# Performance work log

Measured on AMD Instinct MI355X. Metric: run time of the kernel, lower is better.

## Reference

```python
import jax, jax.numpy as jnp
import numpy as np

B, T, C = 4, 1024, 2048
H, HKV, HD = 32, 8, 64
HID = 5632  # round_up(8*2048/3, 256)
EPS = 1e-6


def rmsnorm(x, scale):
    return x * scale * jax.lax.rsqrt(jnp.mean(x * x, axis=-1, keepdims=True) + EPS)


def rotary(t, cos, sin):
    # interleaved even/odd rotation, matching torch apply_rotary_emb
    te, to = t[..., ::2], t[..., 1::2]
    return jnp.stack((te * cos - to * sin, te * sin + to * cos), axis=-1).reshape(t.shape)


def setup_inputs() -> dict:
    key = jax.random.key(0)
    ks = jax.random.split(key, 8)
    s = 0.02
    inv = 1.0 / (10000.0 ** (np.arange(0, HD, 2, dtype=np.float64) / HD))
    ang = np.arange(T, dtype=np.float64)[:, None] * inv[None, :]
    return {
        "x": jax.random.normal(ks[0], (B, T, C), jnp.float32),
        "cos": jnp.asarray(np.cos(ang), jnp.float32),
        "sin": jnp.asarray(np.sin(ang), jnp.float32),
        "w_attn": jax.random.normal(ks[1], (C, (H + 2 * HKV) * HD), jnp.float32) * s,
        "w_proj": jax.random.normal(ks[2], (C, C), jnp.float32) * s,
        "w_gate": jax.random.normal(ks[3], (C, HID), jnp.float32) * s,
        "w_up": jax.random.normal(ks[4], (C, HID), jnp.float32) * s,
        "w_down": jax.random.normal(ks[5], (HID, C), jnp.float32) * s,
        "scale1": jnp.ones((C,), jnp.float32),
        "scale2": jnp.ones((C,), jnp.float32),
    }


def reference(x, cos, sin, w_attn, w_proj, w_gate, w_up, w_down, scale1, scale2):
    n_rep = H // HKV
    # --- attention block ---
    h = rmsnorm(x, scale1)
    qkv = h @ w_attn  # [B,T,(H+2*HKV)*HD]
    q, k, v = jnp.split(qkv, [H * HD, (H + HKV) * HD], axis=-1)
    q = q.reshape(B, T, H, HD).transpose(0, 2, 1, 3)      # [B,H,T,HD]
    k = k.reshape(B, T, HKV, HD).transpose(0, 2, 1, 3)    # [B,HKV,T,HD]
    v = v.reshape(B, T, HKV, HD).transpose(0, 2, 1, 3)
    q = rotary(q, cos, sin)
    k = rotary(k, cos, sin)
    # GQA: group q heads over kv heads instead of repeat_interleave
    qg = q.reshape(B, HKV, n_rep, T, HD)
    scores = jnp.einsum('bgrtd,bgsd->bgrts', qg, k) / jnp.sqrt(jnp.float32(HD))
    causal = jnp.tril(jnp.ones((T, T), bool))
    scores = jnp.where(causal, scores, jnp.finfo(scores.dtype).min)
    p = jax.nn.softmax(scores, axis=-1)
    y = jnp.einsum('bgrts,bgsd->bgrtd', p, v)
    y = y.reshape(B, H, T, HD).transpose(0, 2, 1, 3).reshape(B, T, C)
    x = x + y @ w_proj
    # --- SwiGLU MLP block ---
    h2 = rmsnorm(x, scale2)
    x = x + (jax.nn.silu(h2 @ w_gate) * (h2 @ w_up)) @ w_down
    return x
```

## Files before the change

### kernel.cpp

```cpp
#include <hip/hip_runtime.h>
#include <stdint.h>

#define B_ 4
#define T_ 1024
#define C_ 2048
#define H_ 32
#define HKV_ 8
#define HD_ 64
#define HID_ 5632

typedef __attribute__((ext_vector_type(8))) short short8;
typedef __attribute__((ext_vector_type(4))) float floatx4;

__device__ __forceinline__ float b2f(short s) {
  unsigned u = ((unsigned)(unsigned short)s) << 16;
  return __uint_as_float(u);
}
__device__ __forceinline__ short f2b(float f) {
  unsigned u = __float_as_uint(f);
  u = u + 0x7fffu + ((u >> 16) & 1u);
  return (short)(u >> 16);
}

#define GL2LDS(gp, lp)                                              \
  __builtin_amdgcn_global_load_lds(                                 \
      (const __attribute__((address_space(1))) void*)(gp),          \
      (__attribute__((address_space(3))) void*)(lp), 16, 0, 0)

__global__ __launch_bounds__(256) void convt_kernel(
    const float* __restrict__ W, short* __restrict__ Wt, int K, int N) {
  __shared__ short t[32][33];
  int n0 = blockIdx.x * 32, k0 = blockIdx.y * 32;
  int tx = threadIdx.x & 31, ty = threadIdx.x >> 5;
#pragma unroll
  for (int j = 0; j < 4; ++j)
    t[ty + j * 8][tx] = f2b(W[(size_t)(k0 + ty + j * 8) * N + n0 + tx]);
  __syncthreads();
#pragma unroll
  for (int j = 0; j < 4; ++j)
    Wt[(size_t)(n0 + ty + j * 8) * K + k0 + tx] = t[tx][ty + j * 8];
}

__global__ __launch_bounds__(256) void rmsnorm_kernel(
    const float* __restrict__ x, const float* __restrict__ scale,
    short* __restrict__ out) {
  int row = blockIdx.x, tid = threadIdx.x;
  const float4* xr = (const float4*)(x + (size_t)row * C_);
  float4 v0 = xr[tid], v1 = xr[tid + 256];
  float s = v0.x * v0.x + v0.y * v0.y + v0.z * v0.z + v0.w * v0.w +
            v1.x * v1.x + v1.y * v1.y + v1.z * v1.z + v1.w * v1.w;
  for (int off = 32; off > 0; off >>= 1) s += __shfl_down(s, off, 64);
  __shared__ float red[4];
  if ((tid & 63) == 0) red[tid >> 6] = s;
  __syncthreads();
  float tot = red[0] + red[1] + red[2] + red[3];
  float r = rsqrtf(tot * (1.0f / (float)C_) + 1e-6f);
  const float4* sc = (const float4*)scale;
  float4 s0 = sc[tid], s1 = sc[tid + 256];
  short* o = out + (size_t)row * C_;
  o[tid * 4 + 0] = f2b(v0.x * s0.x * r);
  o[tid * 4 + 1] = f2b(v0.y * s0.y * r);
  o[tid * 4 + 2] = f2b(v0.z * s0.z * r);
  o[tid * 4 + 3] = f2b(v0.w * s0.w * r);
  o[1024 + tid * 4 + 0] = f2b(v1.x * s1.x * r);
  o[1024 + tid * 4 + 1] = f2b(v1.y * s1.y * r);
  o[1024 + tid * 4 + 2] = f2b(v1.z * s1.z * r);
  o[1024 + tid * 4 + 3] = f2b(v1.w * s1.w * r);
}

template <int EPI>
__global__ __launch_bounds__(256, 2) void gemm128_kernel(
    const short* __restrict__ A, const short* __restrict__ Bt,
    void* __restrict__ Out, const float* __restrict__ resid,
    int M, int N, int K) {
  __shared__ __align__(16) short smem[8192];
  short* As = smem;
  short* Bs = smem + 4096;
  int tid = threadIdx.x, lane = tid & 63, wave = tid >> 6;
  int quad = lane >> 4, l16 = lane & 15;
  int m0 = blockIdx.y * 128, n0 = blockIdx.x * 128;
  int wm = (wave & 1) * 64, wn = (wave >> 1) * 64;

  int SA0 = wave * 128 + lane, SA1 = SA0 + 64;
  int rA0 = SA0 >> 2, kA0 = ((SA0 & 3) - ((SA0 >> 3) & 3)) & 3;
  int rA1 = SA1 >> 2, kA1 = ((SA1 & 3) - ((SA1 >> 3) & 3)) & 3;
  const short* ap0 = A + (size_t)(m0 + rA0) * K + kA0 * 8;
  const short* ap1 = A + (size_t)(m0 + rA1) * K + kA1 * 8;
  const short* bp0 = Bt + (size_t)(n0 + rA0) * K + kA0 * 8;
  const short* bp1 = Bt + (size_t)(n0 + rA1) * K + kA1 * 8;
  short* lA0 = As + (wave * 128) * 8;
  short* lA1 = As + (wave * 128 + 64) * 8;
  short* lB0 = Bs + (wave * 128) * 8;
  short* lB1 = Bs + (wave * 128 + 64) * 8;

  int aoff[4], boff[4];
#pragma unroll
  for (int i = 0; i < 4; ++i) {
    int ra = wm + i * 16 + l16;
    aoff[i] = (ra * 4 + ((quad + (ra >> 1)) & 3)) * 8;
    int rb = wn + i * 16 + l16;
    boff[i] = (rb * 4 + ((quad + (rb >> 1)) & 3)) * 8;
  }

  floatx4 acc[4][4] = {};
  for (int k0 = 0; k0 < K; k0 += 32) {
    GL2LDS(ap0 + k0, lA0);
    GL2LDS(ap1 + k0, lA1);
    GL2LDS(bp0 + k0, lB0);
    GL2LDS(bp1 + k0, lB1);
    __syncthreads();
    short8 af[4], bf[4];
#pragma unroll
    for (int i = 0; i < 4; ++i) af[i] = *(const short8*)(As + aoff[i]);
#pragma unroll
    for (int i = 0; i < 4; ++i) bf[i] = *(const short8*)(Bs + boff[i]);
#pragma unroll
    for (int mi = 0; mi < 4; ++mi)
#pragma unroll
      for (int ni = 0; ni < 4; ++ni)
        acc[mi][ni] = __builtin_amdgcn_mfma_f32_16x16x32_bf16(
            af[mi], bf[ni], acc[mi][ni], 0, 0, 0);
    __syncthreads();
  }
#pragma unroll
  for (int mi = 0; mi < 4; ++mi)
#pragma unroll
    for (int ni = 0; ni < 4; ++ni)
#pragma unroll
      for (int r = 0; r < 4; ++r) {
        int row = m0 + wm + mi * 16 + quad * 4 + r;
        int col = n0 + wn + ni * 16 + l16;
        size_t idx = (size_t)row * N + col;
        float a = acc[mi][ni][r];
        if constexpr (EPI == 0)
          ((short*)Out)[idx] = f2b(a);
        else
          ((float*)Out)[idx] = resid[idx] + a;
      }
}

__global__ __launch_bounds__(256, 2) void gateup_kernel(
    const short* __restrict__ A, const short* __restrict__ Wg,
    const short* __restrict__ Wu, short* __restrict__ act, int K) {
  __shared__ __align__(16) short smem[8192];
  short* As = smem;
  short* Bs = smem + 4096;
  int tid = threadIdx.x, lane = tid & 63, wave = tid >> 6;
  int quad = lane >> 4, l16 = lane & 15;
  int m0 = blockIdx.y * 128, n0 = blockIdx.x * 64;
  int wm = (wave & 1) * 64, half = wave >> 1;

  int SA0 = wave * 128 + lane, SA1 = SA0 + 64;
  int rA0 = SA0 >> 2, kA0 = ((SA0 & 3) - ((SA0 >> 3) & 3)) & 3;
  int rA1 = SA1 >> 2, kA1 = ((SA1 & 3) - ((SA1 >> 3) & 3)) & 3;
  const short* ap0 = A + (size_t)(m0 + rA0) * K + kA0 * 8;
  const short* ap1 = A + (size_t)(m0 + rA1) * K + kA1 * 8;
  const short* bp0 = (rA0 < 64 ? Wg + (size_t)(n0 + rA0) * K
                               : Wu + (size_t)(n0 + rA0 - 64) * K) + kA0 * 8;
  const short* bp1 = (rA1 < 64 ? Wg + (size_t)(n0 + rA1) * K
                               : Wu + (size_t)(n0 + rA1 - 64) * K) + kA1 * 8;
  short* lA0 = As + (wave * 128) * 8;
  short* lA1 = As + (wave * 128 + 64) * 8;
  short* lB0 = Bs + (wave * 128) * 8;
  short* lB1 = Bs + (wave * 128 + 64) * 8;

  int aoff[4], boff[4];
#pragma unroll
  for (int i = 0; i < 4; ++i) {
    int ra = wm + i * 16 + l16;
    aoff[i] = (ra * 4 + ((quad + (ra >> 1)) & 3)) * 8;
    int rb = half * 64 + i * 16 + l16;
    boff[i] = (rb * 4 + ((quad + (rb >> 1)) & 3)) * 8;
  }

  floatx4 acc[4][4] = {};
  for (int k0 = 0; k0 < K; k0 += 32) {
    GL2LDS(ap0 + k0, lA0);
    GL2LDS(ap1 + k0, lA1);
    GL2LDS(bp0 + k0, lB0);
    GL2LDS(bp1 + k0, lB1);
    __syncthreads();
    short8 af[4], bf[4];
#pragma unroll
    for (int i = 0; i < 4; ++i) af[i] = *(const short8*)(As + aoff[i]);
#pragma unroll
    for (int i = 0; i < 4; ++i) bf[i] = *(const short8*)(Bs + boff[i]);
#pragma unroll
    for (int mi = 0; mi < 4; ++mi)
#pragma unroll
      for (int ni = 0; ni < 4; ++ni)
        acc[mi][ni] = __builtin_amdgcn_mfma_f32_16x16x32_bf16(
            af[mi], bf[ni], acc[mi][ni], 0, 0, 0);
    __syncthreads();
  }
  short* Ex = smem;
  if (half == 1) {
#pragma unroll
    for (int mi = 0; mi < 4; ++mi)
#pragma unroll
      for (int ni = 0; ni < 4; ++ni)
#pragma unroll
        for (int r = 0; r < 4; ++r)
          Ex[(wm + mi * 16 + quad * 4 + r) * 64 + ni * 16 + l16] =
              f2b(acc[mi][ni][r]);
  }
  __syncthreads();
  if (half == 0) {
#pragma unroll
    for (int mi = 0; mi < 4; ++mi)
#pragma unroll
      for (int ni = 0; ni < 4; ++ni)
#pragma unroll
        for (int r = 0; r < 4; ++r) {
          int row = wm + mi * 16 + quad * 4 + r;
          int col = ni * 16 + l16;
          float u = b2f(Ex[row * 64 + col]);
          float g = acc[mi][ni][r];
          float a = g / (1.0f + __expf(-g)) * u;
          act[(size_t)(m0 + row) * HID_ + n0 + col] = f2b(a);
        }
  }
}

__global__ __launch_bounds__(256) void rope_kernel(
    const short* __restrict__ qkv, const float* __restrict__ cosp,
    const float* __restrict__ sinp, short* __restrict__ q,
    short* __restrict__ k, short* __restrict__ v) {
  int idx = blockIdx.x * 256 + threadIdx.x;
  int i = idx & 31;
  int rest = idx >> 5;
  int head = rest % 48;
  int rest2 = rest / 48;
  int t = rest2 & 1023;
  int b = rest2 >> 10;
  const short* src = qkv + (size_t)(b * T_ + t) * 3072 + head * 64 + 2 * i;
  float e = b2f(src[0]), o = b2f(src[1]);
  if (head < 32) {
    float c = cosp[t * 32 + i], s = sinp[t * 32 + i];
    short* dst = q + ((size_t)(b * 32 + head) * 1024 + t) * 64 + 2 * i;
    dst[0] = f2b(e * c - o * s);
    dst[1] = f2b(e * s + o * c);
  } else if (head < 40) {
    float c = cosp[t * 32 + i], s = sinp[t * 32 + i];
    short* dst = k + ((size_t)(b * 8 + (head - 32)) * 1024 + t) * 64 + 2 * i;
    dst[0] = f2b(e * c - o * s);
    dst[1] = f2b(e * s + o * c);
  } else {
    short* dst = v + ((size_t)(b * 8 + (head - 40)) * 1024 + t) * 64 + 2 * i;
    dst[0] = src[0];
    dst[1] = src[1];
  }
}

__global__ __launch_bounds__(256) void attn_kernel(
    const short* __restrict__ q, const short* __restrict__ k,
    const short* __restrict__ v, short* __restrict__ y) {
  __shared__ __align__(16) short P[4][640];
  int bx = blockIdx.x, h = blockIdx.y, b = blockIdx.z;
  int lane = threadIdx.x & 63, wave = threadIdx.x >> 6;
  int quad = lane >> 4, l16 = lane & 15;
  int g = h >> 2;
  const short* qp = q + (size_t)(b * H_ + h) * T_ * HD_;
  const short* kp = k + (size_t)(b * HKV_ + g) * T_ * HD_;
  const short* vp = v + (size_t)(b * HKV_ + g) * T_ * HD_;
  int q0 = bx * 64 + wave * 16;
  short8 qf0 = *(const short8*)(qp + (q0 + l16) * HD_ + quad * 8);
  short8 qf1 = *(const short8*)(qp + (q0 + l16) * HD_ + 32 + quad * 8);
  floatx4 acc[4] = {};
  float m_r[4] = {-1e30f, -1e30f, -1e30f, -1e30f};
  float l_r[4] = {0.f, 0.f, 0.f, 0.f};
  int qi[4];
#pragma unroll
  for (int r = 0; r < 4; ++r) qi[r] = q0 + quad * 4 + r;
  for (int k0 = 0; k0 < q0 + 16; k0 += 32) {
    floatx4 s0 = {0.f, 0.f, 0.f, 0.f}, s1 = {0.f, 0.f, 0.f, 0.f};
    short8 kf0 = *(const short8*)(kp + (k0 + l16) * HD_ + quad * 8);
    short8 kf0b = *(const short8*)(kp + (k0 + l16) * HD_ + 32 + quad * 8);
    s0 = __builtin_amdgcn_mfma_f32_16x16x32_bf16(qf0, kf0, s0, 0, 0, 0);
    s0 = __builtin_amdgcn_mfma_f32_16x16x32_bf16(qf1, kf0b, s0, 0, 0, 0);
    short8 kf1 = *(const short8*)(kp + (k0 + 16 + l16) * HD_ + quad * 8);
    short8 kf1b = *(const short8*)(kp + (k0 + 16 + l16) * HD_ + 32 + quad * 8);
    s1 = __builtin_amdgcn_mfma_f32_16x16x32_bf16(qf0, kf1, s1, 0, 0, 0);
    s1 = __builtin_amdgcn_mfma_f32_16x16x32_bf16(qf1, kf1b, s1, 0, 0, 0);
    float p0[4], p1[4], mt[4];
#pragma unroll
    for (int r = 0; r < 4; ++r) {
      p0[r] = (k0 + l16 <= qi[r]) ? s0[r] * 0.125f : -1e30f;
      p1[r] = (k0 + 16 + l16 <= qi[r]) ? s1[r] * 0.125f : -1e30f;
      mt[r] = fmaxf(p0[r], p1[r]);
    }
#pragma unroll
    for (int off = 1; off < 16; off <<= 1) {
#pragma unroll
      for (int r = 0; r < 4; ++r) mt[r] = fmaxf(mt[r], __shfl_xor(mt[r], off, 64));
    }
    float alpha[4];
#pragma unroll
    for (int r = 0; r < 4; ++r) {
      float mn = fmaxf(m_r[r], mt[r]);
      alpha[r] = __expf(m_r[r] - mn);
      m_r[r] = mn;
      p0[r] = __expf(p0[r] - mn);
      p1[r] = __expf(p1[r] - mn);
    }
    float rs[4];
#pragma unroll
    for (int r = 0; r < 4; ++r) rs[r] = p0[r] + p1[r];
#pragma unroll
    for (int off = 1; off < 16; off <<= 1) {
#pragma unroll
      for (int r = 0; r < 4; ++r) rs[r] += __shfl_xor(rs[r], off, 64);
    }
#pragma unroll
    for (int r = 0; r < 4; ++r) l_r[r] = l_r[r] * alpha[r] + rs[r];
#pragma unroll
    for (int n = 0; n < 4; ++n)
#pragma unroll
      for (int r = 0; r < 4; ++r) acc[n][r] *= alpha[r];
#pragma unroll
    for (int r = 0; r < 4; ++r) {
      P[wave][(quad * 4 + r) * 40 + l16] = f2b(p0[r]);
      P[wave][(quad * 4 + r) * 40 + 16 + l16] = f2b(p1[r]);
    }
    short8 pf = *(const short8*)(&P[wave][l16 * 40 + quad * 8]);
#pragma unroll
    for (int n = 0; n < 4; ++n) {
      short8 vf;
#pragma unroll
      for (int j = 0; j < 8; ++j)
        vf[j] = vp[(size_t)(k0 + quad * 8 + j) * HD_ + n * 16 + l16];
      acc[n] = __builtin_amdgcn_mfma_f32_16x16x32_bf16(pf, vf, acc[n], 0, 0, 0);
    }
  }
#pragma unroll
  for (int n = 0; n < 4; ++n)
#pragma unroll
    for (int r = 0; r < 4; ++r) {
      int t = q0 + quad * 4 + r;
      y[(size_t)(b * T_ + t) * C_ + h * 64 + n * 16 + l16] = f2b(acc[n][r] / l_r[r]);
    }
}

extern "C" void kernel_launch(void* const* d_in, const int* in_sizes, int n_in,
                              void* d_out, int out_size, void* d_ws, size_t ws_size,
                              hipStream_t stream) {
  const float* x = (const float*)d_in[0];
  const float* cosp = (const float*)d_in[1];
  const float* sinp = (const float*)d_in[2];
  const float* w_attn = (const float*)d_in[3];
  const float* w_proj = (const float*)d_in[4];
  const float* w_gate = (const float*)d_in[5];
  const float* w_up = (const float*)d_in[6];
  const float* w_down = (const float*)d_in[7];
  const float* scale1 = (const float*)d_in[8];
  const float* scale2 = (const float*)d_in[9];
  float* out = (float*)d_out;
  char* ws = (char*)d_ws;

  short* S1 = (short*)(ws + 0);
  short* S2 = (short*)(ws + 23068672);
  short* hbuf = (short*)(ws + 46137344);
  short* S0 = (short*)(ws + 62914560);
  short* qkv = (short*)(ws + 75497472);
  short* kbuf = (short*)(ws + 100663296);
  short* vbuf = (short*)(ws + 104857600);
  short* act = (short*)(ws + 62914560);

  convt_kernel<<<dim3(3072 / 32, 2048 / 32), 256, 0, stream>>>(w_attn, S0, 2048, 3072);
  rmsnorm_kernel<<<4096, 256, 0, stream>>>(x, scale1, hbuf);
  gemm128_kernel<0><<<dim3(3072 / 128, 4096 / 128), 256, 0, stream>>>(
      hbuf, S0, qkv, nullptr, 4096, 3072, 2048);
  rope_kernel<<<24576, 256, 0, stream>>>(qkv, cosp, sinp, hbuf, kbuf, vbuf);
  attn_kernel<<<dim3(16, 32, 4), 256, 0, stream>>>(hbuf, kbuf, vbuf, qkv);
  convt_kernel<<<dim3(2048 / 32, 2048 / 32), 256, 0, stream>>>(w_proj, S0, 2048, 2048);
  gemm128_kernel<1><<<dim3(2048 / 128, 4096 / 128), 256, 0, stream>>>(
      qkv, S0, out, x, 4096, 2048, 2048);
  rmsnorm_kernel<<<4096, 256, 0, stream>>>(out, scale2, hbuf);
  convt_kernel<<<dim3(5632 / 32, 2048 / 32), 256, 0, stream>>>(w_gate, S1, 2048, 5632);
  convt_kernel<<<dim3(5632 / 32, 2048 / 32), 256, 0, stream>>>(w_up, S2, 2048, 5632);
  gateup_kernel<<<dim3(5632 / 64, 4096 / 128), 256, 0, stream>>>(hbuf, S1, S2, act, 2048);
  convt_kernel<<<dim3(2048 / 32, 5632 / 32), 256, 0, stream>>>(w_down, S1, 5632, 2048);
  gemm128_kernel<1><<<dim3(2048 / 128, 4096 / 128), 256, 0, stream>>>(
      act, S1, out, out, 4096, 2048, 5632);
}
```

Measured before the change: 901.9 us.

## Double GEMM K-tile to 64, pre-transpose V, fold softmax scale into Q

The GEMM and gate/up kernels now stage a K-depth of 64 per iteration with an 8-way XOR swizzle in LDS, halving the number of barrier pairs per K sweep at the cost of doubled shared memory. A new transpose kernel writes V as [d][t], so the attention PV step can load each V fragment with one 16-byte vector read instead of eight strided scalar loads. The 1/sqrt(HD) scale is applied to Q during rope instead of per score, which adds a bf16 rounding of the scaled Q and one extra launch plus buffer for V transpose.

```diff
diff --git a/kernel.cpp b/kernel.cpp
--- a/kernel.cpp
+++ b/kernel.cpp
@@ -39,6 +39,22 @@
 #pragma unroll
   for (int j = 0; j < 4; ++j)
     Wt[(size_t)(n0 + ty + j * 8) * K + k0 + tx] = t[tx][ty + j * 8];
+}
+
+__global__ __launch_bounds__(256) void vt_kernel(
+    const short* __restrict__ vin, short* __restrict__ vout) {
+  __shared__ short t[32][33];
+  int t0 = blockIdx.x * 32, d0 = blockIdx.y * 32, bg = blockIdx.z;
+  int tx = threadIdx.x & 31, ty = threadIdx.x >> 5;
+  const short* src = vin + (size_t)bg * T_ * HD_;
+  short* dst = vout + (size_t)bg * T_ * HD_;
+#pragma unroll
+  for (int j = 0; j < 4; ++j)
+    t[ty + j * 8][tx] = src[(size_t)(t0 + ty + j * 8) * HD_ + d0 + tx];
+  __syncthreads();
+#pragma unroll
+  for (int j = 0; j < 4; ++j)
+    dst[(size_t)(d0 + ty + j * 8) * T_ + t0 + tx] = t[tx][ty + j * 8];
 }
 
 __global__ __launch_bounds__(256) void rmsnorm_kernel(
@@ -73,53 +89,59 @@
     const short* __restrict__ A, const short* __restrict__ Bt,
     void* __restrict__ Out, const float* __restrict__ resid,
     int M, int N, int K) {
-  __shared__ __align__(16) short smem[8192];
+  __shared__ __align__(16) short smem[16384];
   short* As = smem;
-  short* Bs = smem + 4096;
+  short* Bs = smem + 8192;
   int tid = threadIdx.x, lane = tid & 63, wave = tid >> 6;
   int quad = lane >> 4, l16 = lane & 15;
   int m0 = blockIdx.y * 128, n0 = blockIdx.x * 128;
   int wm = (wave & 1) * 64, wn = (wave >> 1) * 64;
 
-  int SA0 = wave * 128 + lane, SA1 = SA0 + 64;
-  int rA0 = SA0 >> 2, kA0 = ((SA0 & 3) - ((SA0 >> 3) & 3)) & 3;
-  int rA1 = SA1 >> 2, kA1 = ((SA1 & 3) - ((SA1 >> 3) & 3)) & 3;
-  const short* ap0 = A + (size_t)(m0 + rA0) * K + kA0 * 8;
-  const short* ap1 = A + (size_t)(m0 + rA1) * K + kA1 * 8;
-  const short* bp0 = Bt + (size_t)(n0 + rA0) * K + kA0 * 8;
-  const short* bp1 = Bt + (size_t)(n0 + rA1) * K + kA1 * 8;
-  short* lA0 = As + (wave * 128) * 8;
-  short* lA1 = As + (wave * 128 + 64) * 8;
-  short* lB0 = Bs + (wave * 128) * 8;
-  short* lB1 = Bs + (wave * 128 + 64) * 8;
+  const short* ap[4];
+  const short* bp[4];
+  short* lA[4];
+  short* lB[4];
+#pragma unroll
+  for (int c = 0; c < 4; ++c) {
+    int S = wave * 256 + c * 64 + lane;
+    int row = S >> 3, kc = ((S & 7) - (row & 7)) & 7;
+    ap[c] = A + (size_t)(m0 + row) * K + kc * 8;
+    bp[c] = Bt + (size_t)(n0 + row) * K + kc * 8;
+    lA[c] = As + (wave * 256 + c * 64) * 8;
+    lB[c] = Bs + (wave * 256 + c * 64) * 8;
+  }
 
   int aoff[4], boff[4];
 #pragma unroll
   for (int i = 0; i < 4; ++i) {
     int ra = wm + i * 16 + l16;
-    aoff[i] = (ra * 4 + ((quad + (ra >> 1)) & 3)) * 8;
+    aoff[i] = (ra * 8 + ((quad + ra) & 7)) * 8;
     int rb = wn + i * 16 + l16;
-    boff[i] = (rb * 4 + ((quad + (rb >> 1)) & 3)) * 8;
+    boff[i] = (rb * 8 + ((quad + rb) & 7)) * 8;
   }
 
   floatx4 acc[4][4] = {};
-  for (int k0 = 0; k0 < K; k0 += 32) {
-    GL2LDS(ap0 + k0, lA0);
-    GL2LDS(ap1 + k0, lA1);
-    GL2LDS(bp0 + k0, lB0);
-    GL2LDS(bp1 + k0, lB1);
+  for (int k0 = 0; k0 < K; k0 += 64) {
+#pragma unroll
+    for (int c = 0; c < 4; ++c) {
+      GL2LDS(ap[c] + k0, lA[c]);
+      GL2LDS(bp[c] + k0, lB[c]);
+    }
     __syncthreads();
-    short8 af[4], bf[4];
-#pragma unroll
-    for (int i = 0; i < 4; ++i) af[i] = *(const short8*)(As + aoff[i]);
-#pragma unroll
-    for (int i = 0; i < 4; ++i) bf[i] = *(const short8*)(Bs + boff[i]);
-#pragma unroll
-    for (int mi = 0; mi < 4; ++mi)
-#pragma unroll
-      for (int ni = 0; ni < 4; ++ni)
-        acc[mi][ni] = __builtin_amdgcn_mfma_f32_16x16x32_bf16(
-            af[mi], bf[ni], acc[mi][ni], 0, 0, 0);
+#pragma unroll
+    for (int h = 0; h < 2; ++h) {
+      short8 af[4], bf[4];
+#pragma unroll
+      for (int i = 0; i < 4; ++i) af[i] = *(const short8*)(As + (aoff[i] ^ (h * 32)));
+#pragma unroll
+      for (int i = 0; i < 4; ++i) bf[i] = *(const short8*)(Bs + (boff[i] ^ (h * 32)));
+#pragma unroll
+      for (int mi = 0; mi < 4; ++mi)
+#pragma unroll
+        for (int ni = 0; ni < 4; ++ni)
+          acc[mi][ni] = __builtin_amdgcn_mfma_f32_16x16x32_bf16(
+              af[mi], bf[ni], acc[mi][ni], 0, 0, 0);
+    }
     __syncthreads();
   }
 #pragma unroll
@@ -142,55 +164,61 @@
 __global__ __launch_bounds__(256, 2) void gateup_kernel(
     const short* __restrict__ A, const short* __restrict__ Wg,
     const short* __restrict__ Wu, short* __restrict__ act, int K) {
-  __shared__ __align__(16) short smem[8192];
+  __shared__ __align__(16) short smem[16384];
   short* As = smem;
-  short* Bs = smem + 4096;
+  short* Bs = smem + 8192;
   int tid = threadIdx.x, lane = tid & 63, wave = tid >> 6;
   int quad = lane >> 4, l16 = lane & 15;
   int m0 = blockIdx.y * 128, n0 = blockIdx.x * 64;
   int wm = (wave & 1) * 64, half = wave >> 1;
-
-  int SA0 = wave * 128 + lane, SA1 = SA0 + 64;
-  int rA0 = SA0 >> 2, kA0 = ((SA0 & 3) - ((SA0 >> 3) & 3)) & 3;
-  int rA1 = SA1 >> 2, kA1 = ((SA1 & 3) - ((SA1 >> 3) & 3)) & 3;
-  const short* ap0 = A + (size_t)(m0 + rA0) * K + kA0 * 8;
-  const short* ap1 = A + (size_t)(m0 + rA1) * K + kA1 * 8;
-  const short* bp0 = (rA0 < 64 ? Wg + (size_t)(n0 + rA0) * K
-                               : Wu + (size_t)(n0 + rA0 - 64) * K) + kA0 * 8;
-  const short* bp1 = (rA1 < 64 ? Wg + (size_t)(n0 + rA1) * K
-                               : Wu + (size_t)(n0 + rA1 - 64) * K) + kA1 * 8;
-  short* lA0 = As + (wave * 128) * 8;
-  short* lA1 = As + (wave * 128 + 64) * 8;
-  short* lB0 = Bs + (wave * 128) * 8;
-  short* lB1 = Bs + (wave * 128 + 64) * 8;
+  int half_stage = wave >> 1;
+
+  const short* ap[4];
+  const short* bp[4];
+  short* lA[4];
+  short* lB[4];
+  const short* Bsel = half_stage ? Wu : Wg;
+#pragma unroll
+  for (int c = 0; c < 4; ++c) {
+    int S = wave * 256 + c * 64 + lane;
+    int row = S >> 3, kc = ((S & 7) - (row & 7)) & 7;
+    ap[c] = A + (size_t)(m0 + row) * K + kc * 8;
+    bp[c] = Bsel + (size_t)(n0 + row - half_stage * 64) * K + kc * 8;
+    lA[c] = As + (wave * 256 + c * 64) * 8;
+    lB[c] = Bs + (wave * 256 + c * 64) * 8;
+  }
 
   int aoff[4], boff[4];
 #pragma unroll
   for (int i = 0; i < 4; ++i) {
     int ra = wm + i * 16 + l16;
-    aoff[i] = (ra * 4 + ((quad + (ra >> 1)) & 3)) * 8;
+    aoff[i] = (ra * 8 + ((quad + ra) & 7)) * 8;
     int rb = half * 64 + i * 16 + l16;
-    boff[i] = (rb * 4 + ((quad + (rb >> 1)) & 3)) * 8;
+    boff[i] = (rb * 8 + ((quad + rb) & 7)) * 8;
   }
 
   floatx4 acc[4][4] = {};
-  for (int k0 = 0; k0 < K; k0 += 32) {
-    GL2LDS(ap0 + k0, lA0);
-    GL2LDS(ap1 + k0, lA1);
-    GL2LDS(bp0 + k0, lB0);
-    GL2LDS(bp1 + k0, lB1);
+  for (int k0 = 0; k0 < K; k0 += 64) {
+#pragma unroll
+    for (int c = 0; c < 4; ++c) {
+      GL2LDS(ap[c] + k0, lA[c]);
+      GL2LDS(bp[c] + k0, lB[c]);
+    }
     __syncthreads();
-    short8 af[4], bf[4];
-#pragma unroll
-    for (int i = 0; i < 4; ++i) af[i] = *(const short8*)(As + aoff[i]);
-#pragma unroll
-    for (int i = 0; i < 4; ++i) bf[i] = *(const short8*)(Bs + boff[i]);
-#pragma unroll
-    for (int mi = 0; mi < 4; ++mi)
-#pragma unroll
-      for (int ni = 0; ni < 4; ++ni)
-        acc[mi][ni] = __builtin_amdgcn_mfma_f32_16x16x32_bf16(
-            af[mi], bf[ni], acc[mi][ni], 0, 0, 0);
+#pragma unroll
+    for (int h = 0; h < 2; ++h) {
+      short8 af[4], bf[4];
+#pragma unroll
+      for (int i = 0; i < 4; ++i) af[i] = *(const short8*)(As + (aoff[i] ^ (h * 32)));
+#pragma unroll
+      for (int i = 0; i < 4; ++i) bf[i] = *(const short8*)(Bs + (boff[i] ^ (h * 32)));
+#pragma unroll
+      for (int mi = 0; mi < 4; ++mi)
+#pragma unroll
+        for (int ni = 0; ni < 4; ++ni)
+          acc[mi][ni] = __builtin_amdgcn_mfma_f32_16x16x32_bf16(
+              af[mi], bf[ni], acc[mi][ni], 0, 0, 0);
+    }
     __syncthreads();
   }
   short* Ex = smem;
@@ -238,8 +266,8 @@
   if (head < 32) {
     float c = cosp[t * 32 + i], s = sinp[t * 32 + i];
     short* dst = q + ((size_t)(b * 32 + head) * 1024 + t) * 64 + 2 * i;
-    dst[0] = f2b(e * c - o * s);
-    dst[1] = f2b(e * s + o * c);
+    dst[0] = f2b((e * c - o * s) * 0.125f);
+    dst[1] = f2b((e * s + o * c) * 0.125f);
   } else if (head < 40) {
     float c = cosp[t * 32 + i], s = sinp[t * 32 + i];
     short* dst = k + ((size_t)(b * 8 + (head - 32)) * 1024 + t) * 64 + 2 * i;
@@ -254,7 +282,7 @@
 
 __global__ __launch_bounds__(256) void attn_kernel(
     const short* __restrict__ q, const short* __restrict__ k,
-    const short* __restrict__ v, short* __restrict__ y) {
+    const short* __restrict__ vt, short* __restrict__ y) {
   __shared__ __align__(16) short P[4][640];
   int bx = blockIdx.x, h = blockIdx.y, b = blockIdx.z;
   int lane = threadIdx.x & 63, wave = threadIdx.x >> 6;
@@ -262,7 +290,7 @@
   int g = h >> 2;
   const short* qp = q + (size_t)(b * H_ + h) * T_ * HD_;
   const short* kp = k + (size_t)(b * HKV_ + g) * T_ * HD_;
-  const short* vp = v + (size_t)(b * HKV_ + g) * T_ * HD_;
+  const short* vp = vt + (size_t)(b * HKV_ + g) * T_ * HD_;
   int q0 = bx * 64 + wave * 16;
   short8 qf0 = *(const short8*)(qp + (q0 + l16) * HD_ + quad * 8);
   short8 qf1 = *(const short8*)(qp + (q0 + l16) * HD_ + 32 + quad * 8);
@@ -285,8 +313,8 @@
     float p0[4], p1[4], mt[4];
 #pragma unroll
     for (int r = 0; r < 4; ++r) {
-      p0[r] = (k0 + l16 <= qi[r]) ? s0[r] * 0.125f : -1e30f;
-      p1[r] = (k0 + 16 + l16 <= qi[r]) ? s1[r] * 0.125f : -1e30f;
+      p0[r] = (k0 + l16 <= qi[r]) ? s0[r] : -1e30f;
+      p1[r] = (k0 + 16 + l16 <= qi[r]) ? s1[r] : -1e30f;
       mt[r] = fmaxf(p0[r], p1[r]);
     }
 #pragma unroll
@@ -325,10 +353,7 @@
     short8 pf = *(const short8*)(&P[wave][l16 * 40 + quad * 8]);
 #pragma unroll
     for (int n = 0; n < 4; ++n) {
-      short8 vf;
-#pragma unroll
-      for (int j = 0; j < 8; ++j)
-        vf[j] = vp[(size_t)(k0 + quad * 8 + j) * HD_ + n * 16 + l16];
+      short8 vf = *(const short8*)(vp + (size_t)(n * 16 + l16) * T_ + k0 + quad * 8);
       acc[n] = __builtin_amdgcn_mfma_f32_16x16x32_bf16(pf, vf, acc[n], 0, 0, 0);
     }
   }
@@ -364,6 +389,7 @@
   short* qkv = (short*)(ws + 75497472);
   short* kbuf = (short*)(ws + 100663296);
   short* vbuf = (short*)(ws + 104857600);
+  short* vtbuf = (short*)(ws + 109051904);
   short* act = (short*)(ws + 62914560);
 
   convt_kernel<<<dim3(3072 / 32, 2048 / 32), 256, 0, stream>>>(w_attn, S0, 2048, 3072);
@@ -371,7 +397,8 @@
   gemm128_kernel<0><<<dim3(3072 / 128, 4096 / 128), 256, 0, stream>>>(
       hbuf, S0, qkv, nullptr, 4096, 3072, 2048);
   rope_kernel<<<24576, 256, 0, stream>>>(qkv, cosp, sinp, hbuf, kbuf, vbuf);
-  attn_kernel<<<dim3(16, 32, 4), 256, 0, stream>>>(hbuf, kbuf, vbuf, qkv);
+  vt_kernel<<<dim3(32, 2, 32), 256, 0, stream>>>(vbuf, vtbuf);
+  attn_kernel<<<dim3(16, 32, 4), 256, 0, stream>>>(hbuf, kbuf, vtbuf, qkv);
   convt_kernel<<<dim3(2048 / 32, 2048 / 32), 256, 0, stream>>>(w_proj, S0, 2048, 2048);
   gemm128_kernel<1><<<dim3(2048 / 128, 4096 / 128), 256, 0, stream>>>(
       qkv, S0, out, x, 4096, 2048, 2048);
```

Result: no change. 889.9 us (-1.3%).
